# Performance work log

Hardware: AMD Instinct MI355X
Metric: run time of the kernel (lower is better)

The kernel has to match this reference:

```python
import jax, jax.numpy as jnp
import numpy as np

D_MODEL = 1024
NUM_HEADS = 16
D_K = D_MODEL // NUM_HEADS
ROPE_THETA = 10000.0


def apply_rope(x, pos):
    # x: [B, nh, S, d_k], pos: [S]
    d = x.shape[-1]
    inv_freq = ROPE_THETA ** (-jnp.arange(0, d, 2, dtype=jnp.float32) / d)  # [d/2]
    ang = pos.astype(jnp.float32)[:, None] * inv_freq[None, :]              # [S, d/2]
    cos, sin = jnp.cos(ang), jnp.sin(ang)
    x1, x2 = x[..., 0::2], x[..., 1::2]
    out_even = x1 * cos - x2 * sin
    out_odd = x1 * sin + x2 * cos
    return jnp.stack([out_even, out_odd], axis=-1).reshape(x.shape)


def setup_inputs() -> dict:
    key = jax.random.key(0)
    kx, kq, kk, kv, ko = jax.random.split(key, 5)
    B, S = 4, 2048
    std = np.sqrt(2.0 / (D_MODEL + D_MODEL))
    x = jax.random.normal(kx, (B, S, D_MODEL), dtype=jnp.float32)
    q_proj = jax.random.normal(kq, (D_MODEL, D_MODEL), dtype=jnp.float32) * std
    k_proj = jax.random.normal(kk, (D_MODEL, D_MODEL), dtype=jnp.float32) * std
    v_proj = jax.random.normal(kv, (D_MODEL, D_MODEL), dtype=jnp.float32) * std
    o_proj = jax.random.normal(ko, (D_MODEL, D_MODEL), dtype=jnp.float32) * std
    return {"x": x, "q_proj": q_proj, "k_proj": k_proj, "v_proj": v_proj, "o_proj": o_proj}


def reference(x, q_proj, k_proj, v_proj, o_proj):
    B, S, D = x.shape
    nh, dk = NUM_HEADS, D // NUM_HEADS
    # projections: weights stored [d_out, d_in] -> x @ W.T
    def split_heads(t):
        return t.reshape(B, S, nh, dk).transpose(0, 2, 1, 3)  # [B, nh, S, dk]
    q = split_heads(x @ q_proj.T)
    k = split_heads(x @ k_proj.T)
    v = split_heads(x @ v_proj.T)
    pos = jnp.arange(S)
    q = apply_rope(q, pos)
    k = apply_rope(k, pos)
    scores = jnp.einsum('bhqd,bhkd->bhqk', q, k) / jnp.sqrt(jnp.float32(dk))
    causal = jnp.tril(jnp.ones((S, S), dtype=bool))
    scores = jnp.where(causal, scores, -jnp.inf)
    attn = jax.nn.softmax(scores, axis=-1)
    out = jnp.einsum('bhqk,bhkd->bhqd', attn, v)          # [B, nh, S, dk]
    out = out.transpose(0, 2, 1, 3).reshape(B, S, D)      # merge heads
    return out @ o_proj.T
```

## Files before the change

### kernel.cpp

```cpp
#include <hip/hip_runtime.h>
#include <hip/hip_bf16.h>
#include <cstdint>


typedef __attribute__((ext_vector_type(8))) short short8;
typedef __attribute__((ext_vector_type(4))) float float4v;

#define MFMA16(a, b, c) __builtin_amdgcn_mfma_f32_16x16x32_bf16((a), (b), (c), 0, 0, 0)

__device__ __forceinline__ void glds16(const void* g, void* l) {
    __builtin_amdgcn_global_load_lds(
        (const __attribute__((address_space(1))) void*)g,
        (__attribute__((address_space(3))) void*)l, 16, 0, 0);
}

__device__ __forceinline__ unsigned int pk2(float a, float b) {
    __hip_bfloat162 h = __float22bfloat162_rn(make_float2(a, b));
    union { __hip_bfloat162 h; unsigned int u; } v; v.h = h;
    return v.u;
}

__device__ __forceinline__ unsigned short f2bf(float x) {
    union { float f; unsigned int u; } v; v.f = x;
    unsigned int r = (v.u + 0x7FFFu + ((v.u >> 16) & 1u)) >> 16;
    return (unsigned short)r;
}

__device__ __forceinline__ float bf2f(unsigned short b) {
    union { unsigned int u; float f; } v; v.u = ((unsigned int)b) << 16;
    return v.f;
}

__device__ __forceinline__ short8 load8f(const float* p) {
    const float4 f0 = *(const float4*)p;
    const float4 f1 = *(const float4*)(p + 4);
    union { short8 s; unsigned int u[4]; } r;
    r.u[0] = pk2(f0.x, f0.y);
    r.u[1] = pk2(f0.z, f0.w);
    r.u[2] = pk2(f1.x, f1.y);
    r.u[3] = pk2(f1.z, f1.w);
    return r.s;
}

__global__ __launch_bounds__(256) void convert_kernel(
    const float* __restrict__ in, __hip_bfloat16* __restrict__ out)
{
    const int idx = (blockIdx.x * 256 + threadIdx.x) * 8;
    *(short8*)(out + idx) = load8f(in + idx);
}

__global__ __launch_bounds__(256) void rope_table_kernel(float2* __restrict__ table)
{
    const int idx = blockIdx.x * 256 + threadIdx.x;
    const int pos = idx >> 5, fi = idx & 31;
    const float f = exp2f(-(float)fi * (13.287712379549449f / 32.0f));
    float sn, cs;
    sincosf((float)pos * f, &sn, &cs);
    table[idx] = make_float2(cs, sn);
}

__global__ __launch_bounds__(256) void rope_kernel(
    __hip_bfloat16* __restrict__ T, const float2* __restrict__ table, float scale)
{
    const int idx = blockIdx.x * 256 + threadIdx.x;
    const int r = idx >> 9;
    const int p = idx & 511;
    const int h = p >> 5, i = p & 31;
    const float2 cs = table[(r & 2047) * 32 + i];
    unsigned short* ptr = (unsigned short*)T + (int64_t)r * 1024 + h * 64 + 2 * i;
    const ushort2 xv = *(const ushort2*)ptr;
    const float x1 = bf2f(xv.x), x2 = bf2f(xv.y);
    const unsigned int o = pk2((x1 * cs.x - x2 * cs.y) * scale,
                               (x1 * cs.y + x2 * cs.x) * scale);
    *(unsigned int*)ptr = o;
}

template<int BBF>
__global__ __launch_bounds__(256) void qkv_gemm(
    const __hip_bfloat16* __restrict__ Abf,
    const void* __restrict__ Wq, const void* __restrict__ Wk, const void* __restrict__ Wv,
    __hip_bfloat16* __restrict__ Qp, __hip_bfloat16* __restrict__ Kp,
    __hip_bfloat16* __restrict__ Vt)
{
    __shared__ unsigned short smem[128 * 132];

    const int K = 1024;
    const int bm = blockIdx.x / 24, bn = blockIdx.x % 24;
    const int widx = bn >> 3;
    const int bcol0 = (bn & 7) * 128;
    const void* W = (widx == 0) ? Wq : (widx == 1) ? Wk : Wv;

    const int tid = threadIdx.x;
    const int wave = tid >> 6, lane = tid & 63;
    const int wm = (wave >> 1) * 64, wn = (wave & 1) * 64;
    const int m16 = lane & 15, quad = lane >> 4;

    const int lrow = lane >> 2, lcol = (lane & 3) * 8;
    const int srow = tid >> 2, scol = (tid & 3) * 8;

    float4v acc[4][4] = {};

    for (int k0 = 0; k0 < K; k0 += 32) {
        short8 rb0, rb1;
        if (!BBF) {
            const float* Wf = (const float*)W;
            rb0 = load8f(Wf + (int64_t)(bcol0 + srow) * K + scol + k0);
            rb1 = load8f(Wf + (int64_t)(bcol0 + 64 + srow) * K + scol + k0);
        }
        __syncthreads();
        {
            const __hip_bfloat16* g = Abf + (int64_t)(bm * 128 + wave * 32 + lrow) * K + lcol + k0;
            glds16(g, &smem[wave * 1024]);
            glds16(g + (int64_t)16 * K, &smem[wave * 1024 + 512]);
        }
        if (BBF) {
            const __hip_bfloat16* g = (const __hip_bfloat16*)W +
                (int64_t)(bcol0 + wave * 32 + lrow) * K + lcol + k0;
            glds16(g, &smem[4096 + wave * 1024]);
            glds16(g + (int64_t)16 * K, &smem[4096 + wave * 1024 + 512]);
        } else {
            *(short8*)&smem[4096 + srow * 32 + scol] = rb0;
            *(short8*)&smem[4096 + (64 + srow) * 32 + scol] = rb1;
        }
        __syncthreads();

        short8 af[4], bf[4];
#pragma unroll
        for (int i = 0; i < 4; i++)
            af[i] = *(const short8*)&smem[(wm + i * 16 + m16) * 32 + quad * 8];
#pragma unroll
        for (int j = 0; j < 4; j++)
            bf[j] = *(const short8*)&smem[4096 + (wn + j * 16 + m16) * 32 + quad * 8];
#pragma unroll
        for (int i = 0; i < 4; i++)
#pragma unroll
            for (int j = 0; j < 4; j++)
                acc[i][j] = MFMA16(af[i], bf[j], acc[i][j]);
    }

    if (widx == 2) {
        __syncthreads();
#pragma unroll
        for (int i = 0; i < 4; i++)
#pragma unroll
            for (int j = 0; j < 4; j++)
#pragma unroll
                for (int r = 0; r < 4; r++)
                    smem[(wn + j * 16 + m16) * 132 + wm + i * 16 + quad * 4 + r] =
                        f2bf(acc[i][j][r]);
        __syncthreads();
        const int dc = tid >> 4;
        const int seg = (tid & 15) * 8;
#pragma unroll
        for (int pass = 0; pass < 8; pass++) {
            const int dcol = pass * 16 + dc;
            const short8 v = *(const short8*)&smem[dcol * 132 + seg];
            *(short8*)((unsigned short*)Vt + (int64_t)(bcol0 + dcol) * 8192 + bm * 128 + seg) = v;
        }
    } else {
        __hip_bfloat16* dst = (widx == 0) ? Qp : Kp;
        const int row0 = bm * 128 + wm + quad * 4;
        const int col0 = bcol0 + wn + m16;
#pragma unroll
        for (int i = 0; i < 4; i++)
#pragma unroll
            for (int j = 0; j < 4; j++)
#pragma unroll
                for (int r = 0; r < 4; r++)
                    dst[(int64_t)(row0 + i * 16 + r) * 1024 + col0 + j * 16] =
                        __float2bfloat16(acc[i][j][r]);
    }
}

template<int BBF>
__global__ __launch_bounds__(256) void gemm_o(
    const __hip_bfloat16* __restrict__ Abf, const void* __restrict__ B,
    float* __restrict__ C, int M, int N, int K)
{
    __shared__ __hip_bfloat16 lA[128 * 32];
    __shared__ __hip_bfloat16 lB[128 * 32];

    const int nb = N >> 7;
    const int bm = blockIdx.x / nb, bn = blockIdx.x % nb;
    const int tid = threadIdx.x;
    const int wave = tid >> 6, lane = tid & 63;
    const int wm = (wave >> 1) * 64, wn = (wave & 1) * 64;
    const int m16 = lane & 15, quad = lane >> 4;
    const int lrow = lane >> 2, lcol = (lane & 3) * 8;
    const int srow = tid >> 2, scol = (tid & 3) * 8;

    float4v acc[4][4] = {};

    for (int k0 = 0; k0 < K; k0 += 32) {
        short8 rb0, rb1;
        if (!BBF) {
            const float* Bf = (const float*)B;
            rb0 = load8f(Bf + (int64_t)(bn * 128 + srow) * K + scol + k0);
            rb1 = load8f(Bf + (int64_t)(bn * 128 + 64 + srow) * K + scol + k0);
        }
        __syncthreads();
        {
            const __hip_bfloat16* g = Abf + (int64_t)(bm * 128 + wave * 32 + lrow) * K + lcol + k0;
            glds16(g, &lA[wave * 1024]);
            glds16(g + (int64_t)16 * K, &lA[wave * 1024 + 512]);
        }
        if (BBF) {
            const __hip_bfloat16* g = (const __hip_bfloat16*)B +
                (int64_t)(bn * 128 + wave * 32 + lrow) * K + lcol + k0;
            glds16(g, &lB[wave * 1024]);
            glds16(g + (int64_t)16 * K, &lB[wave * 1024 + 512]);
        } else {
            *(short8*)&lB[srow * 32 + scol] = rb0;
            *(short8*)&lB[(64 + srow) * 32 + scol] = rb1;
        }
        __syncthreads();

        short8 af[4], bf[4];
#pragma unroll
        for (int i = 0; i < 4; i++)
            af[i] = *(const short8*)&lA[(wm + i * 16 + m16) * 32 + quad * 8];
#pragma unroll
        for (int j = 0; j < 4; j++)
            bf[j] = *(const short8*)&lB[(wn + j * 16 + m16) * 32 + quad * 8];
#pragma unroll
        for (int i = 0; i < 4; i++)
#pragma unroll
            for (int j = 0; j < 4; j++)
                acc[i][j] = MFMA16(af[i], bf[j], acc[i][j]);
    }

    const int row0 = bm * 128 + wm + quad * 4;
    const int col0 = bn * 128 + wn + m16;
#pragma unroll
    for (int i = 0; i < 4; i++)
#pragma unroll
        for (int j = 0; j < 4; j++)
#pragma unroll
            for (int r = 0; r < 4; r++)
                C[(int64_t)(row0 + i * 16 + r) * N + col0 + j * 16] = acc[i][j][r];
}

__global__ __launch_bounds__(256) void attn_kernel(
    const __hip_bfloat16* __restrict__ Q,
    const __hip_bfloat16* __restrict__ Kg,
    const __hip_bfloat16* __restrict__ Vt,
    __hip_bfloat16* __restrict__ O,
    int S, int BS)
{
    const int g = blockIdx.x >> 6;
    const int qt = (g < 4) ? 15 - g : (g < 8) ? 11 - g : (g < 12) ? g : g - 12;
    const int bh = blockIdx.x & 63;
    const int b = bh >> 4, h = bh & 15;
    const int tid = threadIdx.x;
    const int wave = tid >> 6, lane = tid & 63;
    const int m16 = lane & 15, quad = lane >> 4;

    __shared__ __hip_bfloat16 lK[64 * 64];
    __shared__ __hip_bfloat16 lV[64 * 64];
    __shared__ __hip_bfloat16 lP[4][32 * 64];

    const int qrow0 = qt * 128 + wave * 32;
    const int64_t rowbase = (int64_t)b * S;

    short8 aq[2][2];
#pragma unroll
    for (int i = 0; i < 2; i++) {
        const __hip_bfloat16* qp = Q + (rowbase + qrow0 + i * 16 + m16) * 1024 + h * 64 + quad * 8;
        aq[i][0] = *(const short8*)qp;
        aq[i][1] = *(const short8*)(qp + 32);
    }

    float lsum[2] = {0.f, 0.f};
    float4v o_acc[2][4] = {};

    const int srow = tid >> 3;
    const int scol = (tid & 7) * 8;

    const int ktmax_blk = 2 * qt + 1;
    const int ktmax_w = 2 * qt + (wave >> 1);
    const int k8 = (m16 & 7) * 8;

    short8 pk0, pk1, pv0, pv1;
#define PREFETCH(KT)                                                                          \
    do {                                                                                      \
        pk0 = *(const short8*)(Kg + (rowbase + (KT) * 64 + srow) * 1024 + h * 64 + scol);     \
        pk1 = *(const short8*)(Kg + (rowbase + (KT) * 64 + srow + 32) * 1024 + h * 64 + scol);\
        pv0 = *(const short8*)(Vt + (int64_t)(h * 64 + srow) * BS + rowbase + (KT) * 64 + scol);      \
        pv1 = *(const short8*)(Vt + (int64_t)(h * 64 + srow + 32) * BS + rowbase + (KT) * 64 + scol); \
    } while (0)

    PREFETCH(0);

    for (int kt = 0; kt <= ktmax_blk; kt++) {
        __syncthreads();
        *(short8*)&lK[srow * 64 + (scol ^ ((srow & 7) * 8))] = pk0;
        *(short8*)&lK[(srow + 32) * 64 + (scol ^ (((srow + 32) & 7) * 8))] = pk1;
        *(short8*)&lV[srow * 64 + (scol ^ ((srow & 7) * 8))] = pv0;
        *(short8*)&lV[(srow + 32) * 64 + (scol ^ (((srow + 32) & 7) * 8))] = pv1;
        __syncthreads();

        if (kt < ktmax_blk) PREFETCH(kt + 1);

        if (kt <= ktmax_w) {
            float4v st[4][2] = {};
#pragma unroll
            for (int mi = 0; mi < 4; mi++) {
                const int n = mi * 16 + m16;
                const int sw = (n & 7) * 8;
                short8 k0 = *(const short8*)&lK[n * 64 + ((quad * 8) ^ sw)];
                short8 k1 = *(const short8*)&lK[n * 64 + ((32 + quad * 8) ^ sw)];
#pragma unroll
                for (int ni = 0; ni < 2; ni++) {
                    st[mi][ni] = MFMA16(k0, aq[ni][0], st[mi][ni]);
                    st[mi][ni] = MFMA16(k1, aq[ni][1], st[mi][ni]);
                }
            }

            const bool need_mask = (kt * 64 + 63 > qrow0);
#pragma unroll
            for (int ni = 0; ni < 2; ni++) {
                const int qg = qrow0 + ni * 16 + m16;
#pragma unroll
                for (int mi = 0; mi < 4; mi++) {
                    float p[4];
#pragma unroll
                    for (int r = 0; r < 4; r++) {
                        p[r] = exp2f(st[mi][ni][r]);
                        if (need_mask) {
                            const int kvg = kt * 64 + mi * 16 + quad * 4 + r;
                            if (kvg > qg) p[r] = 0.0f;
                        }
                    }
                    lsum[ni] += (p[0] + p[1]) + (p[2] + p[3]);
                    uint2 w;
                    w.x = pk2(p[0], p[1]);
                    w.y = pk2(p[2], p[3]);
                    *(uint2*)&lP[wave][(ni * 16 + m16) * 64 + ((mi * 16 + quad * 4) ^ k8)] = w;
                }
            }

            short8 ap[2][2];
#pragma unroll
            for (int i = 0; i < 2; i++)
#pragma unroll
                for (int ks = 0; ks < 2; ks++)
                    ap[i][ks] = *(const short8*)
                        &lP[wave][(i * 16 + m16) * 64 + ((ks * 32 + quad * 8) ^ k8)];
#pragma unroll
            for (int jd = 0; jd < 4; jd++) {
                const int d = jd * 16 + m16;
                const int sw = (d & 7) * 8;
                short8 b0 = *(const short8*)&lV[d * 64 + ((quad * 8) ^ sw)];
                short8 b1 = *(const short8*)&lV[d * 64 + ((32 + quad * 8) ^ sw)];
#pragma unroll
                for (int i = 0; i < 2; i++) {
                    o_acc[i][jd] = MFMA16(ap[i][0], b0, o_acc[i][jd]);
                    o_acc[i][jd] = MFMA16(ap[i][1], b1, o_acc[i][jd]);
                }
            }
        }
    }
#undef PREFETCH

    float rinv[2];
#pragma unroll
    for (int ni = 0; ni < 2; ni++) {
        float v = lsum[ni];
        v += __shfl_xor(v, 16);
        v += __shfl_xor(v, 32);
        rinv[ni] = 1.0f / v;
    }
    float ri[2][4];
#pragma unroll
    for (int i = 0; i < 2; i++)
#pragma unroll
        for (int r = 0; r < 4; r++)
            ri[i][r] = __shfl(rinv[i], quad * 4 + r);

#pragma unroll
    for (int i = 0; i < 2; i++)
#pragma unroll
        for (int jd = 0; jd < 4; jd++)
#pragma unroll
            for (int r = 0; r < 4; r++) {
                const int row = qrow0 + i * 16 + quad * 4 + r;
                O[(rowbase + row) * 1024 + h * 64 + jd * 16 + m16] =
                    __float2bfloat16(o_acc[i][jd][r] * ri[i][r]);
            }
}

extern "C" void kernel_launch(void* const* d_in, const int* in_sizes, int n_in,
                              void* d_out, int out_size, void* d_ws, size_t ws_size,
                              hipStream_t stream)
{
    const float* x  = (const float*)d_in[0];
    const float* qw = (const float*)d_in[1];
    const float* kw = (const float*)d_in[2];
    const float* vw = (const float*)d_in[3];
    const float* ow = (const float*)d_in[4];

    const int BS = 8192, D = 1024, S = 2048;
    const size_t MiB = 1024 * 1024;

    char* ws = (char*)d_ws;
    __hip_bfloat16* xb  = (__hip_bfloat16*)(ws);
    __hip_bfloat16* Qb  = (__hip_bfloat16*)(ws + 16 * MiB);
    __hip_bfloat16* Kb  = (__hip_bfloat16*)(ws + 32 * MiB);
    __hip_bfloat16* Vtb = (__hip_bfloat16*)(ws + 48 * MiB);
    __hip_bfloat16* wqb = (__hip_bfloat16*)(ws + 64 * MiB);
    __hip_bfloat16* wkb = (__hip_bfloat16*)(ws + 66 * MiB);
    __hip_bfloat16* wvb = (__hip_bfloat16*)(ws + 68 * MiB);
    __hip_bfloat16* wob = (__hip_bfloat16*)(ws + 70 * MiB);
    float2* table = (float2*)(ws);
    const bool wbf = ws_size >= 72 * MiB;

    dim3 blk(256);
    convert_kernel<<<(BS * D) / 2048, blk, 0, stream>>>(x, xb);
    if (wbf) {
        convert_kernel<<<(D * D) / 2048, blk, 0, stream>>>(qw, wqb);
        convert_kernel<<<(D * D) / 2048, blk, 0, stream>>>(kw, wkb);
        convert_kernel<<<(D * D) / 2048, blk, 0, stream>>>(vw, wvb);
        convert_kernel<<<(D * D) / 2048, blk, 0, stream>>>(ow, wob);
        qkv_gemm<1><<<64 * 24, blk, 0, stream>>>(xb, wqb, wkb, wvb, Qb, Kb, Vtb);
    } else {
        qkv_gemm<0><<<64 * 24, blk, 0, stream>>>(xb, qw, kw, vw, Qb, Kb, Vtb);
    }
    rope_table_kernel<<<256, blk, 0, stream>>>(table);
    rope_kernel<<<(BS * 512) / 256, blk, 0, stream>>>(Qb, table, 0.18033688011112042f);
    rope_kernel<<<(BS * 512) / 256, blk, 0, stream>>>(Kb, table, 1.0f);
    attn_kernel<<<4 * 16 * (S / 128), blk, 0, stream>>>(Qb, Kb, Vtb, Qb , S, BS);
    if (wbf) gemm_o<1><<<(BS / 128) * (D / 128), blk, 0, stream>>>(Qb, wob, (float*)d_out, BS, D, D);
    else     gemm_o<0><<<(BS / 128) * (D / 128), blk, 0, stream>>>(Qb, ow,  (float*)d_out, BS, D, D);
}
```

Measured before the change: 295.1 us.

## Merge small launches, retile output GEMM, swizzle V transpose, MFMA row sums

Merges the four weight-convert launches into one kernel and the two RoPE launches into one, cutting launch overhead. Narrows the output-projection GEMM tile from 128x128 to 128x64, doubling the block count. Replaces the padded V-transpose staging buffer with an XOR-swizzled layout and adds occupancy hints to the QKV and attention kernels. In attention, the softmax row sums are computed by an MFMA against a vector of ones, replacing scalar adds and shuffles; this adds MFMA work and sums the bf16-rounded probabilities.

```diff
diff --git a/kernel.cpp b/kernel.cpp
--- a/kernel.cpp
+++ b/kernel.cpp
@@ -49,6 +49,19 @@
     *(short8*)(out + idx) = load8f(in + idx);
 }
 
+__global__ __launch_bounds__(256) void convert4_kernel(
+    const float* __restrict__ a, const float* __restrict__ b,
+    const float* __restrict__ c, const float* __restrict__ d,
+    __hip_bfloat16* __restrict__ oa, __hip_bfloat16* __restrict__ ob,
+    __hip_bfloat16* __restrict__ oc, __hip_bfloat16* __restrict__ od)
+{
+    const int m = blockIdx.x >> 9;
+    const float* in = (m == 0) ? a : (m == 1) ? b : (m == 2) ? c : d;
+    __hip_bfloat16* out = (m == 0) ? oa : (m == 1) ? ob : (m == 2) ? oc : od;
+    const int idx = ((blockIdx.x & 511) * 256 + threadIdx.x) * 8;
+    *(short8*)(out + idx) = load8f(in + idx);
+}
+
 __global__ __launch_bounds__(256) void rope_table_kernel(float2* __restrict__ table)
 {
     const int idx = blockIdx.x * 256 + threadIdx.x;
@@ -59,10 +72,14 @@
     table[idx] = make_float2(cs, sn);
 }
 
-__global__ __launch_bounds__(256) void rope_kernel(
-    __hip_bfloat16* __restrict__ T, const float2* __restrict__ table, float scale)
-{
-    const int idx = blockIdx.x * 256 + threadIdx.x;
+__global__ __launch_bounds__(256) void rope2_kernel(
+    __hip_bfloat16* __restrict__ Qp, __hip_bfloat16* __restrict__ Kp,
+    const float2* __restrict__ table)
+{
+    const int sel = blockIdx.x >> 14;
+    __hip_bfloat16* T = sel ? Kp : Qp;
+    const float scale = sel ? 1.0f : 0.18033688011112042f;
+    const int idx = (blockIdx.x & 16383) * 256 + threadIdx.x;
     const int r = idx >> 9;
     const int p = idx & 511;
     const int h = p >> 5, i = p & 31;
@@ -76,13 +93,13 @@
 }
 
 template<int BBF>
-__global__ __launch_bounds__(256) void qkv_gemm(
+__global__ __launch_bounds__(256, 5) void qkv_gemm(
     const __hip_bfloat16* __restrict__ Abf,
     const void* __restrict__ Wq, const void* __restrict__ Wk, const void* __restrict__ Wv,
     __hip_bfloat16* __restrict__ Qp, __hip_bfloat16* __restrict__ Kp,
     __hip_bfloat16* __restrict__ Vt)
 {
-    __shared__ unsigned short smem[128 * 132];
+    __shared__ unsigned short smem[128 * 128];
 
     const int K = 1024;
     const int bm = blockIdx.x / 24, bn = blockIdx.x % 24;
@@ -143,18 +160,22 @@
 #pragma unroll
         for (int i = 0; i < 4; i++)
 #pragma unroll
-            for (int j = 0; j < 4; j++)
-#pragma unroll
-                for (int r = 0; r < 4; r++)
-                    smem[(wn + j * 16 + m16) * 132 + wm + i * 16 + quad * 4 + r] =
-                        f2bf(acc[i][j][r]);
+            for (int j = 0; j < 4; j++) {
+                const int col = wn + j * 16 + m16;
+                const int key = (col & 7) * 8;
+#pragma unroll
+                for (int r = 0; r < 4; r++) {
+                    const int row = wm + i * 16 + quad * 4 + r;
+                    smem[col * 128 + (row ^ key)] = f2bf(acc[i][j][r]);
+                }
+            }
         __syncthreads();
         const int dc = tid >> 4;
         const int seg = (tid & 15) * 8;
 #pragma unroll
         for (int pass = 0; pass < 8; pass++) {
             const int dcol = pass * 16 + dc;
-            const short8 v = *(const short8*)&smem[dcol * 132 + seg];
+            const short8 v = *(const short8*)&smem[dcol * 128 + (seg ^ ((dcol & 7) * 8))];
             *(short8*)((unsigned short*)Vt + (int64_t)(bcol0 + dcol) * 8192 + bm * 128 + seg) = v;
         }
     } else {
@@ -178,25 +199,24 @@
     float* __restrict__ C, int M, int N, int K)
 {
     __shared__ __hip_bfloat16 lA[128 * 32];
-    __shared__ __hip_bfloat16 lB[128 * 32];
-
-    const int nb = N >> 7;
+    __shared__ __hip_bfloat16 lB[64 * 32];
+
+    const int nb = N >> 6;
     const int bm = blockIdx.x / nb, bn = blockIdx.x % nb;
     const int tid = threadIdx.x;
     const int wave = tid >> 6, lane = tid & 63;
-    const int wm = (wave >> 1) * 64, wn = (wave & 1) * 64;
+    const int wm = (wave >> 1) * 64, wn = (wave & 1) * 32;
     const int m16 = lane & 15, quad = lane >> 4;
     const int lrow = lane >> 2, lcol = (lane & 3) * 8;
     const int srow = tid >> 2, scol = (tid & 3) * 8;
 
-    float4v acc[4][4] = {};
+    float4v acc[4][2] = {};
 
     for (int k0 = 0; k0 < K; k0 += 32) {
-        short8 rb0, rb1;
+        short8 rb0;
         if (!BBF) {
             const float* Bf = (const float*)B;
-            rb0 = load8f(Bf + (int64_t)(bn * 128 + srow) * K + scol + k0);
-            rb1 = load8f(Bf + (int64_t)(bn * 128 + 64 + srow) * K + scol + k0);
+            rb0 = load8f(Bf + (int64_t)(bn * 64 + srow) * K + scol + k0);
         }
         __syncthreads();
         {
@@ -206,41 +226,42 @@
         }
         if (BBF) {
             const __hip_bfloat16* g = (const __hip_bfloat16*)B +
-                (int64_t)(bn * 128 + wave * 32 + lrow) * K + lcol + k0;
-            glds16(g, &lB[wave * 1024]);
-            glds16(g + (int64_t)16 * K, &lB[wave * 1024 + 512]);
+                (int64_t)(bn * 64 + wave * 16 + lrow / 1 % 16) * K + lcol + k0;
+            glds16((const __hip_bfloat16*)B +
+                   (int64_t)(bn * 64 + wave * 16 + (lane >> 2)) * K + lcol + k0,
+                   &lB[wave * 512]);
+            (void)g;
         } else {
             *(short8*)&lB[srow * 32 + scol] = rb0;
-            *(short8*)&lB[(64 + srow) * 32 + scol] = rb1;
-        }
-        __syncthreads();
-
-        short8 af[4], bf[4];
+        }
+        __syncthreads();
+
+        short8 af[4], bf[2];
 #pragma unroll
         for (int i = 0; i < 4; i++)
             af[i] = *(const short8*)&lA[(wm + i * 16 + m16) * 32 + quad * 8];
 #pragma unroll
-        for (int j = 0; j < 4; j++)
+        for (int j = 0; j < 2; j++)
             bf[j] = *(const short8*)&lB[(wn + j * 16 + m16) * 32 + quad * 8];
 #pragma unroll
         for (int i = 0; i < 4; i++)
 #pragma unroll
-            for (int j = 0; j < 4; j++)
+            for (int j = 0; j < 2; j++)
                 acc[i][j] = MFMA16(af[i], bf[j], acc[i][j]);
     }
 
     const int row0 = bm * 128 + wm + quad * 4;
-    const int col0 = bn * 128 + wn + m16;
+    const int col0 = bn * 64 + wn + m16;
 #pragma unroll
     for (int i = 0; i < 4; i++)
 #pragma unroll
-        for (int j = 0; j < 4; j++)
+        for (int j = 0; j < 2; j++)
 #pragma unroll
             for (int r = 0; r < 4; r++)
                 C[(int64_t)(row0 + i * 16 + r) * N + col0 + j * 16] = acc[i][j][r];
 }
 
-__global__ __launch_bounds__(256) void attn_kernel(
+__global__ __launch_bounds__(256, 5) void attn_kernel(
     const __hip_bfloat16* __restrict__ Q,
     const __hip_bfloat16* __restrict__ Kg,
     const __hip_bfloat16* __restrict__ Vt,
@@ -270,7 +291,8 @@
         aq[i][1] = *(const short8*)(qp + 32);
     }
 
-    float lsum[2] = {0.f, 0.f};
+    const short8 ones8 = {16256, 16256, 16256, 16256, 16256, 16256, 16256, 16256};
+    float4v lacc[2] = {};
     float4v o_acc[2][4] = {};
 
     const int srow = tid >> 3;
@@ -331,7 +353,6 @@
                             if (kvg > qg) p[r] = 0.0f;
                         }
                     }
-                    lsum[ni] += (p[0] + p[1]) + (p[2] + p[3]);
                     uint2 w;
                     w.x = pk2(p[0], p[1]);
                     w.y = pk2(p[2], p[3]);
@@ -347,6 +368,11 @@
                     ap[i][ks] = *(const short8*)
                         &lP[wave][(i * 16 + m16) * 64 + ((ks * 32 + quad * 8) ^ k8)];
 #pragma unroll
+            for (int i = 0; i < 2; i++) {
+                lacc[i] = MFMA16(ap[i][0], ones8, lacc[i]);
+                lacc[i] = MFMA16(ap[i][1], ones8, lacc[i]);
+            }
+#pragma unroll
             for (int jd = 0; jd < 4; jd++) {
                 const int d = jd * 16 + m16;
                 const int sw = (d & 7) * 8;
@@ -362,20 +388,12 @@
     }
 #undef PREFETCH
 
-    float rinv[2];
-#pragma unroll
-    for (int ni = 0; ni < 2; ni++) {
-        float v = lsum[ni];
-        v += __shfl_xor(v, 16);
-        v += __shfl_xor(v, 32);
-        rinv[ni] = 1.0f / v;
-    }
     float ri[2][4];
 #pragma unroll
     for (int i = 0; i < 2; i++)
 #pragma unroll
         for (int r = 0; r < 4; r++)
-            ri[i][r] = __shfl(rinv[i], quad * 4 + r);
+            ri[i][r] = 1.0f / lacc[i][r];
 
 #pragma unroll
     for (int i = 0; i < 2; i++)
@@ -417,18 +435,15 @@
     dim3 blk(256);
     convert_kernel<<<(BS * D) / 2048, blk, 0, stream>>>(x, xb);
     if (wbf) {
-        convert_kernel<<<(D * D) / 2048, blk, 0, stream>>>(qw, wqb);
-        convert_kernel<<<(D * D) / 2048, blk, 0, stream>>>(kw, wkb);
-        convert_kernel<<<(D * D) / 2048, blk, 0, stream>>>(vw, wvb);
-        convert_kernel<<<(D * D) / 2048, blk, 0, stream>>>(ow, wob);
+        convert4_kernel<<<4 * (D * D) / 2048, blk, 0, stream>>>(
+            qw, kw, vw, ow, wqb, wkb, wvb, wob);
         qkv_gemm<1><<<64 * 24, blk, 0, stream>>>(xb, wqb, wkb, wvb, Qb, Kb, Vtb);
     } else {
         qkv_gemm<0><<<64 * 24, blk, 0, stream>>>(xb, qw, kw, vw, Qb, Kb, Vtb);
     }
     rope_table_kernel<<<256, blk, 0, stream>>>(table);
-    rope_kernel<<<(BS * 512) / 256, blk, 0, stream>>>(Qb, table, 0.18033688011112042f);
-    rope_kernel<<<(BS * 512) / 256, blk, 0, stream>>>(Kb, table, 1.0f);
+    rope2_kernel<<<2 * 16384, blk, 0, stream>>>(Qb, Kb, table);
     attn_kernel<<<4 * 16 * (S / 128), blk, 0, stream>>>(Qb, Kb, Vtb, Qb , S, BS);
-    if (wbf) gemm_o<1><<<(BS / 128) * (D / 128), blk, 0, stream>>>(Qb, wob, (float*)d_out, BS, D, D);
-    else     gemm_o<0><<<(BS / 128) * (D / 128), blk, 0, stream>>>(Qb, ow,  (float*)d_out, BS, D, D);
-}
+    if (wbf) gemm_o<1><<<(BS / 128) * (D / 64), blk, 0, stream>>>(Qb, wob, (float*)d_out, BS, D, D);
+    else     gemm_o<0><<<(BS / 128) * (D / 64), blk, 0, stream>>>(Qb, ow,  (float*)d_out, BS, D, D);
+}
```

Measured after the change: 457.9 us. +55.1%, slower.
